# Kernel tuning notes

Hardware: AMD Instinct MI355X
Metric: run time of the kernel (lower is better)

Reference implementation:

```python
import jax, jax.numpy as jnp
import numpy as np
from jax import lax

T, B, I, H = 512, 128, 256, 1024


def setup_inputs() -> dict:
    key = jax.random.key(0)
    ks = jax.random.split(key, 7)
    s_ih = 1.0 / np.sqrt(H)
    return {
        "inputs": jax.random.normal(ks[0], (T, B, I), dtype=jnp.float32),
        "h0": jax.random.normal(ks[1], (B, H), dtype=jnp.float32),
        "c0": jax.random.normal(ks[2], (B, H), dtype=jnp.float32),
        "W_ih": jax.random.uniform(ks[3], (4 * H, I), dtype=jnp.float32, minval=-s_ih, maxval=s_ih),
        "W_hh": jax.random.uniform(ks[4], (4 * H, H), dtype=jnp.float32, minval=-s_ih, maxval=s_ih),
        "b_ih": jax.random.uniform(ks[5], (4 * H,), dtype=jnp.float32, minval=-s_ih, maxval=s_ih),
        "b_hh": jax.random.uniform(ks[6], (4 * H,), dtype=jnp.float32, minval=-s_ih, maxval=s_ih),
    }


def reference(inputs, h0, c0, W_ih, W_hh, b_ih, b_hh):
    # Precompute input projections for all timesteps in one big GEMM.
    # [T, B, 4H]
    x_proj = jnp.einsum('tbi,gi->tbg', inputs, W_ih) + b_ih + b_hh
    hidden = W_hh.shape[1]

    def step(carry, xp):
        h, c = carry
        gates = xp + h @ W_hh.T  # [B, 4H]
        i_g, f_g, g_g, o_g = jnp.split(gates, 4, axis=-1)
        i_g = jax.nn.sigmoid(i_g)
        f_g = jax.nn.sigmoid(f_g)
        g_g = jnp.tanh(g_g)
        o_g = jax.nn.sigmoid(o_g)
        c_new = f_g * c + i_g * g_g
        h_new = o_g * jnp.tanh(c_new)
        return (h_new, c_new), h_new

    (h_final, c_final), outputs = lax.scan(step, (h0, c0), x_proj)
    # outputs: [T, B, H]; matches torch stack over dim 0 (batch_first=False)
    return outputs, h_final, c_final
```

## Files before the change

### kernel.cpp

```cpp
#include <hip/hip_runtime.h>


#define T_STEPS 512
#define BATCH   128
#define IN_DIM  256
#define HID     1024
#define GATES   4096
#define KDIM    1280

typedef __bf16 bf16x8 __attribute__((ext_vector_type(8)));
typedef float  f32x4  __attribute__((ext_vector_type(4)));

__device__ __forceinline__ unsigned short f2bf(float f) {
  unsigned int u = __builtin_bit_cast(unsigned int, f);
  unsigned int r = (u + 0x7FFFu + ((u >> 16) & 1u)) >> 16;
  return (unsigned short)r;
}

__global__ void cast_weights(const float* __restrict__ Wih,
                             const float* __restrict__ Whh,
                             unsigned short* __restrict__ Wbf) {
  int gid = blockIdx.x * blockDim.x + threadIdx.x;
  if (gid >= GATES * (KDIM / 4)) return;
  int n  = gid / (KDIM / 4);
  int k4 = (gid % (KDIM / 4)) * 4;
  float4 v;
  if (k4 < IN_DIM) v = *reinterpret_cast<const float4*>(Wih + (size_t)n * IN_DIM + k4);
  else             v = *reinterpret_cast<const float4*>(Whh + (size_t)n * HID + (k4 - IN_DIM));
  ushort4 o;
  o.x = f2bf(v.x); o.y = f2bf(v.y); o.z = f2bf(v.z); o.w = f2bf(v.w);
  *reinterpret_cast<ushort4*>(Wbf + (size_t)n * KDIM + k4) = o;
}

__global__ void init_state(const float* __restrict__ h0, const float* __restrict__ c0,
                           const float* __restrict__ bih, const float* __restrict__ bhh,
                           unsigned short* __restrict__ hbf0, float* __restrict__ cws,
                           float* __restrict__ bsum) {
  int i = blockIdx.x * blockDim.x + threadIdx.x;
  if (i < BATCH * HID) { hbf0[i] = f2bf(h0[i]); cws[i] = c0[i]; }
  if (i < GATES) bsum[i] = bih[i] + bhh[i];
}

__global__ __launch_bounds__(256) void lstm_step(
    const float* __restrict__ x_t,
    const unsigned short* __restrict__ Wbf,
    const float* __restrict__ bsum,
    const unsigned short* __restrict__ h_in,
    unsigned short* __restrict__ h_out,
    float* __restrict__ c_ws,
    float* __restrict__ out_t)
{
  __shared__ __align__(16) unsigned short As[64][72];
  __shared__ __align__(16) unsigned short Bs[32][72];
  __shared__ __align__(16) float Gs[64][36];

  const int tid  = threadIdx.x;
  const int cg   = blockIdx.x;
  const int rg   = blockIdx.y;
  const int row0 = rg * 64;
  const int j0   = cg * 8;

  const int wave = tid >> 6;
  const int lane = tid & 63;
  const int col  = lane & 15;
  const int quad = lane >> 4;
  const int mrow = wave * 16 + col;

  f32x4 acc0 = {0.f, 0.f, 0.f, 0.f};
  f32x4 acc1 = {0.f, 0.f, 0.f, 0.f};

  const int wrow = tid >> 3;
  const int kcB  = tid & 7;
  const int gB = wrow >> 3, jjB = wrow & 7;
  const unsigned short* wsrc =
      Wbf + (size_t)(gB * HID + j0 + jjB) * KDIM + kcB * 8;

  for (int kt = 0; kt < KDIM / 64; ++kt) {
    const int kbase = kt * 64;
    #pragma unroll
    for (int p = 0; p < 2; ++p) {
      int idx = p * 256 + tid;
      int row = idx >> 3;
      int kc  = idx & 7;
      int k   = kbase + kc * 8;
      if (k < IN_DIM) {
        const float* src = x_t + (size_t)(row0 + row) * IN_DIM + k;
        float4 f0 = *reinterpret_cast<const float4*>(src);
        float4 f1 = *reinterpret_cast<const float4*>(src + 4);
        ushort4 u0, u1;
        u0.x = f2bf(f0.x); u0.y = f2bf(f0.y); u0.z = f2bf(f0.z); u0.w = f2bf(f0.w);
        u1.x = f2bf(f1.x); u1.y = f2bf(f1.y); u1.z = f2bf(f1.z); u1.w = f2bf(f1.w);
        *reinterpret_cast<ushort4*>(&As[row][kc * 8])     = u0;
        *reinterpret_cast<ushort4*>(&As[row][kc * 8 + 4]) = u1;
      } else {
        const unsigned short* src = h_in + (size_t)(row0 + row) * HID + (k - IN_DIM);
        *reinterpret_cast<uint4*>(&As[row][kc * 8]) =
            *reinterpret_cast<const uint4*>(src);
      }
    }
    *reinterpret_cast<uint4*>(&Bs[wrow][kcB * 8]) =
        *reinterpret_cast<const uint4*>(wsrc + kbase);
    __syncthreads();

    #pragma unroll
    for (int s = 0; s < 2; ++s) {
      bf16x8 a  = *reinterpret_cast<const bf16x8*>(&As[mrow][s * 32 + quad * 8]);
      bf16x8 b0 = *reinterpret_cast<const bf16x8*>(&Bs[col][s * 32 + quad * 8]);
      bf16x8 b1 = *reinterpret_cast<const bf16x8*>(&Bs[16 + col][s * 32 + quad * 8]);
      acc0 = __builtin_amdgcn_mfma_f32_16x16x32_bf16(a, b0, acc0, 0, 0, 0);
      acc1 = __builtin_amdgcn_mfma_f32_16x16x32_bf16(a, b1, acc1, 0, 0, 0);
    }
    __syncthreads();
  }

  #pragma unroll
  for (int r = 0; r < 4; ++r) {
    Gs[wave * 16 + quad * 4 + r][col]      = acc0[r];
    Gs[wave * 16 + quad * 4 + r][16 + col] = acc1[r];
  }
  __syncthreads();

  #pragma unroll
  for (int p = 0; p < 2; ++p) {
    int idx = p * 256 + tid;
    int row = idx >> 3;
    int jj  = idx & 7;
    float ig = Gs[row][jj]      + bsum[j0 + jj];
    float fg = Gs[row][8 + jj]  + bsum[HID + j0 + jj];
    float gg = Gs[row][16 + jj] + bsum[2 * HID + j0 + jj];
    float og = Gs[row][24 + jj] + bsum[3 * HID + j0 + jj];
    ig = 1.f / (1.f + __expf(-ig));
    fg = 1.f / (1.f + __expf(-fg));
    og = 1.f / (1.f + __expf(-og));
    gg = tanhf(gg);
    int b = row0 + row;
    int j = j0 + jj;
    size_t off = (size_t)b * HID + j;
    float c_old = c_ws[off];
    float c_new = fg * c_old + ig * gg;
    float h     = og * tanhf(c_new);
    c_ws[off]  = c_new;
    out_t[off] = h;
    h_out[off] = f2bf(h);
  }
}

__global__ void finalize(const float* __restrict__ c_ws, float* __restrict__ out) {
  int i = blockIdx.x * blockDim.x + threadIdx.x;
  if (i < BATCH * HID) {
    const size_t base = (size_t)T_STEPS * BATCH * HID;
    out[base + i] = out[(size_t)(T_STEPS - 1) * BATCH * HID + i];
    out[base + BATCH * HID + i] = c_ws[i];
  }
}

extern "C" void kernel_launch(void* const* d_in, const int* in_sizes, int n_in,
                              void* d_out, int out_size, void* d_ws, size_t ws_size,
                              hipStream_t stream) {
  const float* x   = (const float*)d_in[0];
  const float* h0  = (const float*)d_in[1];
  const float* c0  = (const float*)d_in[2];
  const float* Wih = (const float*)d_in[3];
  const float* Whh = (const float*)d_in[4];
  const float* bih = (const float*)d_in[5];
  const float* bhh = (const float*)d_in[6];
  float* out = (float*)d_out;

  char* ws = (char*)d_ws;
  unsigned short* Wbf  = (unsigned short*)ws;
  float*          bsum = (float*)(ws + 10485760);
  unsigned short* hbf  = (unsigned short*)(ws + 10485760 + 16384);
  float*          cws  = (float*)(ws + 10485760 + 16384 + 524288);

  cast_weights<<<dim3((GATES * (KDIM / 4) + 255) / 256), 256, 0, stream>>>(Wih, Whh, Wbf);
  init_state<<<dim3((BATCH * HID + 255) / 256), 256, 0, stream>>>(h0, c0, bih, bhh,
                                                                  hbf, cws, bsum);
  for (int t = 0; t < T_STEPS; ++t) {
    lstm_step<<<dim3(128, 2), 256, 0, stream>>>(
        x + (size_t)t * BATCH * IN_DIM, Wbf, bsum,
        hbf + (size_t)(t & 1) * BATCH * HID,
        hbf + (size_t)((t + 1) & 1) * BATCH * HID,
        cws, out + (size_t)t * BATCH * HID);
  }
  finalize<<<dim3((BATCH * HID + 255) / 256), 256, 0, stream>>>(cws, out);
}
```

Baseline: 9.191 ms.

## Replace per-timestep launches with persistent cooperative LSTM kernel using grid sync

Replaces the 512 per-step kernel launches with one cooperative persistent kernel of 256 blocks that loops over timesteps and synchronises with grid.sync(). Each block keeps its 32-row weight slice resident in LDS for all steps and holds the cell state and biases in registers. A operands are read straight from global memory instead of being staged through LDS. This removes launch overhead and repeated weight reloads, at the cost of a grid-wide barrier per step, uncoalesced direct A loads, and reliance on all blocks being co-resident.

```diff
diff --git a/kernel.cpp b/kernel.cpp
--- a/kernel.cpp
+++ b/kernel.cpp
@@ -1,4 +1,7 @@
 #include <hip/hip_runtime.h>
+#include <hip/hip_cooperative_groups.h>
+
+namespace cg = cooperative_groups;
 
 
 #define T_STEPS 512
@@ -8,8 +11,9 @@
 #define GATES   4096
 #define KDIM    1280
 
-typedef __bf16 bf16x8 __attribute__((ext_vector_type(8)));
-typedef float  f32x4  __attribute__((ext_vector_type(4)));
+typedef __bf16          bf16x8 __attribute__((ext_vector_type(8)));
+typedef unsigned short  u16x8  __attribute__((ext_vector_type(8)));
+typedef float           f32x4  __attribute__((ext_vector_type(4)));
 
 __device__ __forceinline__ unsigned short f2bf(float f) {
   unsigned int u = __builtin_bit_cast(unsigned int, f);
@@ -32,126 +36,155 @@
   *reinterpret_cast<ushort4*>(Wbf + (size_t)n * KDIM + k4) = o;
 }
 
-__global__ void init_state(const float* __restrict__ h0, const float* __restrict__ c0,
-                           const float* __restrict__ bih, const float* __restrict__ bhh,
-                           unsigned short* __restrict__ hbf0, float* __restrict__ cws,
+__global__ void init_state(const float* __restrict__ h0,
+                           const float* __restrict__ bih,
+                           const float* __restrict__ bhh,
+                           unsigned short* __restrict__ hbf0,
                            float* __restrict__ bsum) {
   int i = blockIdx.x * blockDim.x + threadIdx.x;
-  if (i < BATCH * HID) { hbf0[i] = f2bf(h0[i]); cws[i] = c0[i]; }
+  if (i < BATCH * HID) hbf0[i] = f2bf(h0[i]);
   if (i < GATES) bsum[i] = bih[i] + bhh[i];
 }
 
-__global__ __launch_bounds__(256) void lstm_step(
-    const float* __restrict__ x_t,
+__global__ __launch_bounds__(256) void lstm_persistent(
+    const float* __restrict__ x,
     const unsigned short* __restrict__ Wbf,
     const float* __restrict__ bsum,
-    const unsigned short* __restrict__ h_in,
-    unsigned short* __restrict__ h_out,
-    float* __restrict__ c_ws,
-    float* __restrict__ out_t)
+    const float* __restrict__ c0,
+    unsigned short* __restrict__ hbf,
+    float* __restrict__ out)
 {
-  __shared__ __align__(16) unsigned short As[64][72];
-  __shared__ __align__(16) unsigned short Bs[32][72];
+  __shared__ __align__(16) unsigned short Bs[32][1288];
   __shared__ __align__(16) float Gs[64][36];
 
   const int tid  = threadIdx.x;
-  const int cg   = blockIdx.x;
-  const int rg   = blockIdx.y;
+  const int bid  = blockIdx.x;
+  const int cg_  = bid & 127;
+  const int rg   = bid >> 7;
   const int row0 = rg * 64;
-  const int j0   = cg * 8;
-
-  const int wave = tid >> 6;
-  const int lane = tid & 63;
-  const int col  = lane & 15;
-  const int quad = lane >> 4;
-  const int mrow = wave * 16 + col;
-
-  f32x4 acc0 = {0.f, 0.f, 0.f, 0.f};
-  f32x4 acc1 = {0.f, 0.f, 0.f, 0.f};
-
-  const int wrow = tid >> 3;
-  const int kcB  = tid & 7;
-  const int gB = wrow >> 3, jjB = wrow & 7;
-  const unsigned short* wsrc =
-      Wbf + (size_t)(gB * HID + j0 + jjB) * KDIM + kcB * 8;
-
-  for (int kt = 0; kt < KDIM / 64; ++kt) {
-    const int kbase = kt * 64;
-    #pragma unroll
-    for (int p = 0; p < 2; ++p) {
-      int idx = p * 256 + tid;
-      int row = idx >> 3;
-      int kc  = idx & 7;
-      int k   = kbase + kc * 8;
-      if (k < IN_DIM) {
-        const float* src = x_t + (size_t)(row0 + row) * IN_DIM + k;
-        float4 f0 = *reinterpret_cast<const float4*>(src);
-        float4 f1 = *reinterpret_cast<const float4*>(src + 4);
-        ushort4 u0, u1;
-        u0.x = f2bf(f0.x); u0.y = f2bf(f0.y); u0.z = f2bf(f0.z); u0.w = f2bf(f0.w);
-        u1.x = f2bf(f1.x); u1.y = f2bf(f1.y); u1.z = f2bf(f1.z); u1.w = f2bf(f1.w);
-        *reinterpret_cast<ushort4*>(&As[row][kc * 8])     = u0;
-        *reinterpret_cast<ushort4*>(&As[row][kc * 8 + 4]) = u1;
-      } else {
-        const unsigned short* src = h_in + (size_t)(row0 + row) * HID + (k - IN_DIM);
-        *reinterpret_cast<uint4*>(&As[row][kc * 8]) =
-            *reinterpret_cast<const uint4*>(src);
+  const int j0   = cg_ * 8;
+
+  const int wave  = tid >> 6;
+  const int lane  = tid & 63;
+  const int col   = lane & 15;
+  const int quad  = lane >> 4;
+  const int quad8 = quad * 8;
+  const int mrow  = wave * 16 + col;
+  const int arow  = row0 + mrow;
+
+  {
+    const int wrow = tid >> 3;
+    const int kcB  = tid & 7;
+    const int gB = wrow >> 3, jjB = wrow & 7;
+    const unsigned short* wsrc =
+        Wbf + (size_t)(gB * HID + j0 + jjB) * KDIM + kcB * 8;
+    #pragma unroll
+    for (int kt = 0; kt < KDIM / 64; ++kt)
+      *reinterpret_cast<uint4*>(&Bs[wrow][kt * 64 + kcB * 8]) =
+          *reinterpret_cast<const uint4*>(wsrc + kt * 64);
+  }
+
+  const int er = tid >> 3;
+  const int jj = tid & 7;
+  const int j  = j0 + jj;
+  const size_t offA = (size_t)(row0 + er) * HID + j;
+  const size_t offB = (size_t)(row0 + er + 32) * HID + j;
+  float cA = c0[offA], cB = c0[offB];
+  float hA = 0.f, hB = 0.f;
+  const float bi  = bsum[j];
+  const float bf_ = bsum[HID + j];
+  const float bg  = bsum[2 * HID + j];
+  const float bo  = bsum[3 * HID + j];
+
+  const unsigned short* Bp0 = &Bs[col][quad8];
+  const unsigned short* Bp1 = &Bs[16 + col][quad8];
+
+  __syncthreads();
+  cg::grid_group grid = cg::this_grid();
+
+  for (int t = 0; t < T_STEPS; ++t) {
+    const unsigned short* hin  = hbf + (size_t)(t & 1) * BATCH * HID;
+    unsigned short*       hout = hbf + (size_t)((t + 1) & 1) * BATCH * HID;
+    const float* xp = x + ((size_t)t * BATCH + arow) * IN_DIM + quad8;
+    const unsigned short* hp = hin + (size_t)arow * HID + quad8;
+
+    f32x4 acc0 = {0.f, 0.f, 0.f, 0.f};
+    f32x4 acc1 = {0.f, 0.f, 0.f, 0.f};
+
+    #pragma unroll
+    for (int kt = 0; kt < 4; ++kt) {
+      #pragma unroll
+      for (int s = 0; s < 2; ++s) {
+        const int k = kt * 64 + s * 32;
+        float4 f0 = *reinterpret_cast<const float4*>(xp + k);
+        float4 f1 = *reinterpret_cast<const float4*>(xp + k + 4);
+        u16x8 u = {f2bf(f0.x), f2bf(f0.y), f2bf(f0.z), f2bf(f0.w),
+                   f2bf(f1.x), f2bf(f1.y), f2bf(f1.z), f2bf(f1.w)};
+        bf16x8 a  = __builtin_bit_cast(bf16x8, u);
+        bf16x8 b0 = *reinterpret_cast<const bf16x8*>(Bp0 + k);
+        bf16x8 b1 = *reinterpret_cast<const bf16x8*>(Bp1 + k);
+        acc0 = __builtin_amdgcn_mfma_f32_16x16x32_bf16(a, b0, acc0, 0, 0, 0);
+        acc1 = __builtin_amdgcn_mfma_f32_16x16x32_bf16(a, b1, acc1, 0, 0, 0);
       }
     }
-    *reinterpret_cast<uint4*>(&Bs[wrow][kcB * 8]) =
-        *reinterpret_cast<const uint4*>(wsrc + kbase);
+    #pragma unroll
+    for (int kt = 4; kt < 20; ++kt) {
+      #pragma unroll
+      for (int s = 0; s < 2; ++s) {
+        const int k = kt * 64 + s * 32;
+        bf16x8 a  = *reinterpret_cast<const bf16x8*>(hp + (k - IN_DIM));
+        bf16x8 b0 = *reinterpret_cast<const bf16x8*>(Bp0 + k);
+        bf16x8 b1 = *reinterpret_cast<const bf16x8*>(Bp1 + k);
+        acc0 = __builtin_amdgcn_mfma_f32_16x16x32_bf16(a, b0, acc0, 0, 0, 0);
+        acc1 = __builtin_amdgcn_mfma_f32_16x16x32_bf16(a, b1, acc1, 0, 0, 0);
+      }
+    }
+
+    #pragma unroll
+    for (int r = 0; r < 4; ++r) {
+      Gs[wave * 16 + quad * 4 + r][col]      = acc0[r];
+      Gs[wave * 16 + quad * 4 + r][16 + col] = acc1[r];
+    }
     __syncthreads();
 
-    #pragma unroll
-    for (int s = 0; s < 2; ++s) {
-      bf16x8 a  = *reinterpret_cast<const bf16x8*>(&As[mrow][s * 32 + quad * 8]);
-      bf16x8 b0 = *reinterpret_cast<const bf16x8*>(&Bs[col][s * 32 + quad * 8]);
-      bf16x8 b1 = *reinterpret_cast<const bf16x8*>(&Bs[16 + col][s * 32 + quad * 8]);
-      acc0 = __builtin_amdgcn_mfma_f32_16x16x32_bf16(a, b0, acc0, 0, 0, 0);
-      acc1 = __builtin_amdgcn_mfma_f32_16x16x32_bf16(a, b1, acc1, 0, 0, 0);
-    }
-    __syncthreads();
+    float* out_t = out + (size_t)t * BATCH * HID;
+    {
+      float ig = Gs[er][jj]      + bi;
+      float fg = Gs[er][8 + jj]  + bf_;
+      float gg = Gs[er][16 + jj] + bg;
+      float og = Gs[er][24 + jj] + bo;
+      ig = 1.f / (1.f + __expf(-ig));
+      fg = 1.f / (1.f + __expf(-fg));
+      og = 1.f / (1.f + __expf(-og));
+      gg = tanhf(gg);
+      cA = fg * cA + ig * gg;
+      hA = og * tanhf(cA);
+      out_t[offA] = hA;
+      hout[offA]  = f2bf(hA);
+    }
+    {
+      float ig = Gs[er + 32][jj]      + bi;
+      float fg = Gs[er + 32][8 + jj]  + bf_;
+      float gg = Gs[er + 32][16 + jj] + bg;
+      float og = Gs[er + 32][24 + jj] + bo;
+      ig = 1.f / (1.f + __expf(-ig));
+      fg = 1.f / (1.f + __expf(-fg));
+      og = 1.f / (1.f + __expf(-og));
+      gg = tanhf(gg);
+      cB = fg * cB + ig * gg;
+      hB = og * tanhf(cB);
+      out_t[offB] = hB;
+      hout[offB]  = f2bf(hB);
+    }
+
+    grid.sync();
   }
 
-  #pragma unroll
-  for (int r = 0; r < 4; ++r) {
-    Gs[wave * 16 + quad * 4 + r][col]      = acc0[r];
-    Gs[wave * 16 + quad * 4 + r][16 + col] = acc1[r];
-  }
-  __syncthreads();
-
-  #pragma unroll
-  for (int p = 0; p < 2; ++p) {
-    int idx = p * 256 + tid;
-    int row = idx >> 3;
-    int jj  = idx & 7;
-    float ig = Gs[row][jj]      + bsum[j0 + jj];
-    float fg = Gs[row][8 + jj]  + bsum[HID + j0 + jj];
-    float gg = Gs[row][16 + jj] + bsum[2 * HID + j0 + jj];
-    float og = Gs[row][24 + jj] + bsum[3 * HID + j0 + jj];
-    ig = 1.f / (1.f + __expf(-ig));
-    fg = 1.f / (1.f + __expf(-fg));
-    og = 1.f / (1.f + __expf(-og));
-    gg = tanhf(gg);
-    int b = row0 + row;
-    int j = j0 + jj;
-    size_t off = (size_t)b * HID + j;
-    float c_old = c_ws[off];
-    float c_new = fg * c_old + ig * gg;
-    float h     = og * tanhf(c_new);
-    c_ws[off]  = c_new;
-    out_t[off] = h;
-    h_out[off] = f2bf(h);
-  }
-}
-
-__global__ void finalize(const float* __restrict__ c_ws, float* __restrict__ out) {
-  int i = blockIdx.x * blockDim.x + threadIdx.x;
-  if (i < BATCH * HID) {
-    const size_t base = (size_t)T_STEPS * BATCH * HID;
-    out[base + i] = out[(size_t)(T_STEPS - 1) * BATCH * HID + i];
-    out[base + BATCH * HID + i] = c_ws[i];
-  }
+  const size_t fin = (size_t)T_STEPS * BATCH * HID;
+  out[fin + offA] = hA;
+  out[fin + BATCH * HID + offA] = cA;
+  out[fin + offB] = hB;
+  out[fin + BATCH * HID + offB] = cB;
 }
 
 extern "C" void kernel_launch(void* const* d_in, const int* in_sizes, int n_in,
@@ -170,17 +203,11 @@
   unsigned short* Wbf  = (unsigned short*)ws;
   float*          bsum = (float*)(ws + 10485760);
   unsigned short* hbf  = (unsigned short*)(ws + 10485760 + 16384);
-  float*          cws  = (float*)(ws + 10485760 + 16384 + 524288);
 
   cast_weights<<<dim3((GATES * (KDIM / 4) + 255) / 256), 256, 0, stream>>>(Wih, Whh, Wbf);
-  init_state<<<dim3((BATCH * HID + 255) / 256), 256, 0, stream>>>(h0, c0, bih, bhh,
-                                                                  hbf, cws, bsum);
-  for (int t = 0; t < T_STEPS; ++t) {
-    lstm_step<<<dim3(128, 2), 256, 0, stream>>>(
-        x + (size_t)t * BATCH * IN_DIM, Wbf, bsum,
-        hbf + (size_t)(t & 1) * BATCH * HID,
-        hbf + (size_t)((t + 1) & 1) * BATCH * HID,
-        cws, out + (size_t)t * BATCH * HID);
-  }
-  finalize<<<dim3((BATCH * HID + 255) / 256), 256, 0, stream>>>(cws, out);
-}
+  init_state<<<dim3((BATCH * HID + 255) / 256), 256, 0, stream>>>(h0, bih, bhh, hbf, bsum);
+
+  void* args[] = {(void*)&x, (void*)&Wbf, (void*)&bsum, (void*)&c0,
+                  (void*)&hbf, (void*)&out};
+  hipLaunchCooperativeKernel(lstm_persistent, dim3(256), dim3(256), args, 0, stream);
+}
```

Result: slower. 20.98 ms (+128.3%).
